# Performance work log

Hardware: AMD Instinct MI355X
Metric: run time of the kernel (lower is better)

The kernel has to match this reference:

```python
import math
import jax, jax.numpy as jnp
import numpy as np

B, N, M, C, H = 64, 64, 64, 512, 8
HD = C // H
FREQ = 256  # frequency_embedding_size
MAX_PERIOD = 10000.0


def setup_inputs() -> dict:
    key = jax.random.key(0)
    ks = jax.random.split(key, 10)
    s = 1.0 / math.sqrt(C)
    sf = 1.0 / math.sqrt(FREQ)
    return {
        "query": jax.random.normal(ks[0], (B, N, C), jnp.float32),
        "query_pos": jax.random.uniform(ks[1], (1, N, M), jnp.float32),
        # projection weights stored as [in, out]
        "Wq": jax.random.normal(ks[2], (C, C), jnp.float32) * s,
        "bq": jnp.zeros((C,), jnp.float32),
        "Wk": jax.random.normal(ks[3], (C, C), jnp.float32) * s,  # no bias
        "Wv": jax.random.normal(ks[4], (C, C), jnp.float32) * s,
        "bv": jnp.zeros((C,), jnp.float32),
        "Wo": jax.random.normal(ks[5], (C, C), jnp.float32) * s,
        "bo": jnp.zeros((C,), jnp.float32),
        # ScalarEmbedder MLP: Linear(FREQ->C), SiLU, Linear(C->C)
        "W1": jax.random.normal(ks[6], (FREQ, C), jnp.float32) * sf,
        "b1": jnp.zeros((C,), jnp.float32),
        "W2": jax.random.normal(ks[7], (C, C), jnp.float32) * s,
        "b2": jnp.zeros((C,), jnp.float32),
    }


def _freqs():
    half = FREQ // 2
    return jnp.exp(-math.log(MAX_PERIOD) * jnp.arange(half, dtype=jnp.float32) / half)


def reference(query, query_pos, Wq, bq, Wk, Wv, bv, Wo, bo, W1, b1, W2, b2):
    Bq, Nq, Cq = query.shape
    Mk = query_pos.shape[-1]
    # --- ScalarEmbedder on flattened pairwise positions: [N*M] -> [N*M, C]
    t = query_pos.reshape(-1)                       # [Bp*N*M], Bp = 1
    tf = t[:, None] * _freqs()[None, :]             # [N*M, FREQ/2]
    emb = jnp.concatenate([jnp.cos(tf), jnp.sin(tf)], axis=-1)  # [N*M, FREQ]
    pe = jax.nn.silu(emb @ W1 + b1) @ W2 + b2        # [N*M, C]
    pe = pe.reshape(Nq, Mk, H, HD).transpose(2, 0, 1, 3)  # [H, N, M, hd] (tiled over B via broadcast)

    q = (query @ Wq + bq).reshape(Bq, Nq, H, HD)     # bnhd
    k = (query @ Wk).reshape(Bq, Mk, H, HD)          # bmhd (key = query)
    v = (query @ Wv + bv).reshape(Bq, Mk, H, HD)

    scale = HD ** -0.5
    # attn[b,h,n,m] = sum_d q[b,n,h,d] * pe[h,n,m,d] * k[b,m,h,d]
    scores = jnp.einsum("bnhd,hnmd,bmhd->bhnm", q, pe, k) * scale
    attn = jax.nn.softmax(scores, axis=-1)
    x = jnp.einsum("bhnm,bmhd->bnhd", attn, v).reshape(Bq, Nq, Cq)
    return x @ Wo + bo + query  # identity = query
```

## Files before the change

kernel.cpp:

```cpp
#include <hip/hip_runtime.h>
#include <hip/hip_bf16.h>
#include <math.h>

typedef short short8 __attribute__((ext_vector_type(8)));
typedef float floatx4 __attribute__((ext_vector_type(4)));

__device__ __forceinline__ ushort f2bf(float f) {
    __hip_bfloat16 h = __float2bfloat16(f);
    return *reinterpret_cast<ushort*>(&h);
}
__device__ __forceinline__ void bf8_to_f32(uint4 u, float* f) {
    f[0] = __uint_as_float(u.x << 16); f[1] = __uint_as_float(u.x & 0xffff0000u);
    f[2] = __uint_as_float(u.y << 16); f[3] = __uint_as_float(u.y & 0xffff0000u);
    f[4] = __uint_as_float(u.z << 16); f[5] = __uint_as_float(u.z & 0xffff0000u);
    f[6] = __uint_as_float(u.w << 16); f[7] = __uint_as_float(u.w & 0xffff0000u);
}

#define GLDS16(g, l) __builtin_amdgcn_global_load_lds( \
    (const __attribute__((address_space(1))) void*)(g), \
    (__attribute__((address_space(3))) void*)(l), 16, 0, 0)

__global__ __launch_bounds__(256) void prep_kernel(
        const float* __restrict__ W1, const float* __restrict__ W2,
        const float* __restrict__ Wq, const float* __restrict__ Wk,
        const float* __restrict__ Wv, const float* __restrict__ Wo,
        const float* __restrict__ bq, const float* __restrict__ bv,
        const float* __restrict__ query, const float* __restrict__ qpos,
        ushort* __restrict__ W1t, ushort* __restrict__ W2t,
        ushort* __restrict__ Wqkvt, ushort* __restrict__ Wot,
        ushort* __restrict__ queryB, ushort* __restrict__ embB,
        float* __restrict__ biasC) {
    const int z = blockIdx.z;
    const int tx = threadIdx.x, ty = threadIdx.y;
    const int tid = ty * 32 + tx;
    if (z < 6) {
        const float* src; ushort* dst; int R;
        switch (z) {
            case 0:  src = W1; dst = W1t;              R = 256; break;
            case 1:  src = W2; dst = W2t;              R = 512; break;
            case 2:  src = Wq; dst = Wqkvt;            R = 512; break;
            case 3:  src = Wk; dst = Wqkvt + 512*512;  R = 512; break;
            case 4:  src = Wv; dst = Wqkvt + 1024*512; R = 512; break;
            default: src = Wo; dst = Wot;              R = 512; break;
        }
        const int r0 = blockIdx.y * 32, c0 = blockIdx.x * 32;
        if (r0 >= R) return;
        __shared__ float t[32][33];
        for (int i = ty; i < 32; i += 8) t[i][tx] = src[(size_t)(r0 + i) * 512 + c0 + tx];
        __syncthreads();
        for (int i = ty; i < 32; i += 8) dst[(size_t)(c0 + i) * R + r0 + tx] = f2bf(t[tx][i]);
    } else if (z == 6) {
        const int bid = blockIdx.y * 16 + blockIdx.x;
#pragma unroll
        for (int i = 0; i < 8; ++i) {
            size_t idx4 = (size_t)bid * 2048 + i * 256 + tid;
            float4 v = *(const float4*)(query + idx4 * 4);
            ushort4 o; o.x = f2bf(v.x); o.y = f2bf(v.y); o.z = f2bf(v.z); o.w = f2bf(v.w);
            *(ushort4*)(queryB + idx4 * 4) = o;
        }
        if (bid == 0) {
            for (int i = tid; i < 1536; i += 256)
                biasC[i] = (i < 512) ? bq[i] : ((i < 1024) ? 0.0f : bv[i - 1024]);
        }
    } else {
        const int bid = blockIdx.y * 16 + blockIdx.x;
        const int gt = bid * 256 + tid;
        const int e0 = gt * 16;
        const int r = e0 >> 8, j0 = e0 & 255;
        const float t = qpos[r];
        ushort o[16];
#pragma unroll
        for (int u = 0; u < 16; ++u) {
            int j = j0 + u, i = j & 127;
            float freq = __expf(-9.210340371976184f * (float)i * (1.0f / 128.0f));
            float a = t * freq;
            o[u] = f2bf((j < 128) ? __cosf(a) : __sinf(a));
        }
        *(uint4*)(embB + e0)     = *(uint4*)&o[0];
        *(uint4*)(embB + e0 + 8) = *(uint4*)&o[8];
    }
}

struct GArgs {
    const ushort* A; const ushort* Bt; const float* bias; const float* resid;
    void* C; int N, K, act, outf32, ntn;
};

template<int BM, int BN>
__global__ __launch_bounds__(256) void gemm_multi(GArgs g0, GArgs g1, int split) {
    constexpr int MR = BM / 32;
    constexpr int NR = BN / 32;
    __shared__ ushort As[2][BM * 32];
    __shared__ ushort Bs[2][BN * 32];

    const bool sel = ((int)blockIdx.x >= split);
    const GArgs g = sel ? g1 : g0;
    const int bid = sel ? ((int)blockIdx.x - split) : (int)blockIdx.x;
    const int tm = bid / g.ntn, tn = bid % g.ntn;
    const int row0 = tm * BM, col0 = tn * BN;
    const int K = g.K, N = g.N;

    const int tid = threadIdx.x;
    const int l = tid & 63, w = tid >> 6;
    const int wr = w >> 1, wc = w & 1;
    const int l15 = l & 15, quad = l >> 4;

    const int srow = tid >> 2;
    const int skoff = (tid & 3) * 8;
    const ushort* gA = g.A  + (size_t)(row0 + srow) * K + skoff;
    const ushort* gB = g.Bt + (size_t)(col0 + srow) * K + skoff;

    auto stage = [&](int s, int k0) {
#pragma unroll
        for (int i = 0; i < BM / 64; ++i)
            GLDS16(gA + (size_t)(i * 64) * K + k0, &As[s][(i * 256 + tid) * 8]);
#pragma unroll
        for (int i = 0; i < BN / 64; ++i)
            GLDS16(gB + (size_t)(i * 64) * K + k0, &Bs[s][(i * 256 + tid) * 8]);
    };

    floatx4 acc[MR][NR] = {};

    const int nk = K >> 5;
    stage(0, 0);
    int cur = 0;
    for (int t = 0; t < nk; ++t) {
        __syncthreads();
        if (t + 1 < nk) stage(cur ^ 1, (t + 1) * 32);
        short8 af[MR], bf[NR];
#pragma unroll
        for (int m = 0; m < MR; ++m)
            af[m] = *(const short8*)&As[cur][(wr * (BM / 2) + m * 16 + l15) * 32 + quad * 8];
#pragma unroll
        for (int n = 0; n < NR; ++n)
            bf[n] = *(const short8*)&Bs[cur][(wc * (BN / 2) + n * 16 + l15) * 32 + quad * 8];
#pragma unroll
        for (int m = 0; m < MR; ++m)
#pragma unroll
            for (int n = 0; n < NR; ++n)
                acc[m][n] = __builtin_amdgcn_mfma_f32_16x16x32_bf16(af[m], bf[n], acc[m][n], 0, 0, 0);
        cur ^= 1;
    }

#pragma unroll
    for (int m = 0; m < MR; ++m)
#pragma unroll
        for (int n = 0; n < NR; ++n) {
            int col = col0 + wc * (BN / 2) + n * 16 + l15;
            float bvv = g.bias ? g.bias[col] : 0.0f;
#pragma unroll
            for (int r = 0; r < 4; ++r) {
                int row = row0 + wr * (BM / 2) + m * 16 + quad * 4 + r;
                float val = acc[m][n][r] + bvv;
                if (g.act) val = val / (1.0f + __expf(-val));
                if (g.outf32) {
                    float rv = g.resid ? g.resid[(size_t)row * N + col] : 0.0f;
                    ((float*)g.C)[(size_t)row * N + col] = val + rv;
                } else {
                    ((ushort*)g.C)[(size_t)row * N + col] = f2bf(val);
                }
            }
        }
}

__global__ __launch_bounds__(256) void attn_bf16(
        const ushort* __restrict__ qkv, const ushort* __restrict__ peB,
        ushort* __restrict__ xB) {
    constexpr int PT = 72;
    const int h = blockIdx.x, b = blockIdx.y, nh = blockIdx.z;
    const int tid = threadIdx.x;
    const int w = tid >> 6, l = tid & 63;
    const int lo = l & 7, hi = l >> 3;
    const int l15 = l & 15, quad = l >> 4;

    __shared__ ushort vsT[64 * PT];
    __shared__ ushort ps[32 * PT];

    {
        const int rp = tid >> 3, ch = tid & 7;
        const ushort* vb = qkv + (size_t)(b * 64 + 2 * rp) * 1536 + h * 64 + 1024 + ch * 8;
        uint4 v0 = *(const uint4*)vb;
        uint4 v1 = *(const uint4*)(vb + 1536);
        const ushort* a0 = (const ushort*)&v0;
        const ushort* a1 = (const ushort*)&v1;
#pragma unroll
        for (int j = 0; j < 8; ++j) {
            uint pk = (uint)a0[j] | ((uint)a1[j] << 16);
            *(uint*)&vsT[(ch * 8 + j) * PT + 2 * rp] = pk;
        }
    }

    short8 ku[8];
#pragma unroll
    for (int mg = 0; mg < 8; ++mg)
        ku[mg] = *(const short8*)(qkv + (size_t)(b * 64 + mg * 8 + hi) * 1536 + h * 64 + 512 + lo * 8);

    for (int i = 0; i < 8; ++i) {
        int nl = w + 4 * i;
        int n = nh * 32 + nl;

        uint4 qu = *(const uint4*)(qkv + (size_t)(b * 64 + n) * 1536 + h * 64 + lo * 8);
        float qf[8]; bf8_to_f32(qu, qf);

        uint4 pu[8];
#pragma unroll
        for (int mg = 0; mg < 8; ++mg)
            pu[mg] = *(const uint4*)(peB + (size_t)(n * 64 + mg * 8 + hi) * 512 + h * 64 + lo * 8);

        float sreg[8];
#pragma unroll
        for (int mg = 0; mg < 8; ++mg) {
            float pf[8]; bf8_to_f32(pu[mg], pf);
            const ushort* kk = (const ushort*)&ku[mg];
            float p = 0.0f;
#pragma unroll
            for (int j = 0; j < 8; ++j) {
                float kfj = __uint_as_float(((uint)kk[j]) << 16);
                p = fmaf(qf[j] * kfj, pf[j], p);
            }
            p += __shfl_xor(p, 1);
            p += __shfl_xor(p, 2);
            p += __shfl_xor(p, 4);
            sreg[mg] = p * 0.125f;
        }

        float mx = sreg[0];
#pragma unroll
        for (int mg = 1; mg < 8; ++mg) mx = fmaxf(mx, sreg[mg]);
        mx = fmaxf(mx, __shfl_xor(mx, 8));
        mx = fmaxf(mx, __shfl_xor(mx, 16));
        mx = fmaxf(mx, __shfl_xor(mx, 32));
        float sum = 0.0f;
#pragma unroll
        for (int mg = 0; mg < 8; ++mg) { sreg[mg] = __expf(sreg[mg] - mx); sum += sreg[mg]; }
        sum += __shfl_xor(sum, 8);
        sum += __shfl_xor(sum, 16);
        sum += __shfl_xor(sum, 32);
        float rs = 1.0f / sum;

        float pv = sreg[0];
#pragma unroll
        for (int mg = 1; mg < 8; ++mg) if (lo == mg) pv = sreg[mg];
        ps[nl * PT + 8 * lo + hi] = f2bf(pv * rs);
    }
    __syncthreads();

    {
        const int ntile = w & 1;
        const int dt0 = (w >> 1) << 1;
        floatx4 o0 = {0.f, 0.f, 0.f, 0.f};
        floatx4 o1 = {0.f, 0.f, 0.f, 0.f};
#pragma unroll
        for (int ks = 0; ks < 2; ++ks) {
            short8 a  = *(const short8*)&ps[(ntile * 16 + l15) * PT + ks * 32 + quad * 8];
            short8 b0 = *(const short8*)&vsT[((dt0    ) * 16 + l15) * PT + ks * 32 + quad * 8];
            short8 b1 = *(const short8*)&vsT[((dt0 + 1) * 16 + l15) * PT + ks * 32 + quad * 8];
            o0 = __builtin_amdgcn_mfma_f32_16x16x32_bf16(a, b0, o0, 0, 0, 0);
            o1 = __builtin_amdgcn_mfma_f32_16x16x32_bf16(a, b1, o1, 0, 0, 0);
        }
        const int nbase = nh * 32 + ntile * 16 + quad * 4;
#pragma unroll
        for (int r = 0; r < 4; ++r) {
            size_t rowoff = (size_t)(b * 64 + nbase + r) * 512 + h * 64;
            xB[rowoff + (dt0    ) * 16 + l15] = f2bf(o0[r]);
            xB[rowoff + (dt0 + 1) * 16 + l15] = f2bf(o1[r]);
        }
    }
}

extern "C" void kernel_launch(void* const* d_in, const int* in_sizes, int n_in,
                              void* d_out, int out_size, void* d_ws, size_t ws_size,
                              hipStream_t stream) {
    const float* query = (const float*)d_in[0];
    const float* qpos  = (const float*)d_in[1];
    const float* Wq    = (const float*)d_in[2];
    const float* bq    = (const float*)d_in[3];
    const float* Wk    = (const float*)d_in[4];
    const float* Wv    = (const float*)d_in[5];
    const float* bv    = (const float*)d_in[6];
    const float* Wo    = (const float*)d_in[7];
    const float* bo    = (const float*)d_in[8];
    const float* W1    = (const float*)d_in[9];
    const float* b1    = (const float*)d_in[10];
    const float* W2    = (const float*)d_in[11];
    const float* b2    = (const float*)d_in[12];
    float* out = (float*)d_out;
    char* ws = (char*)d_ws;

    ushort* W1t    = (ushort*)(ws + 0);
    ushort* W2t    = (ushort*)(ws + 262144);
    ushort* Wqkvt  = (ushort*)(ws + 786432);
    ushort* Wot    = (ushort*)(ws + 2359296);
    float*  biasC  = (float*) (ws + 2883584);
    ushort* embB   = (ushort*)(ws + 3145728);
    ushort* queryB = (ushort*)(ws + 5242880);
    ushort* hiddenB= (ushort*)(ws + 9437184);
    ushort* peB    = (ushort*)(ws + 13631488);
    ushort* qkvB   = (ushort*)(ws + 17825792);
    ushort* xB     = (ushort*)(ws + 30408704);

    prep_kernel<<<dim3(16, 16, 8), dim3(32, 8), 0, stream>>>(
        W1, W2, Wq, Wk, Wv, Wo, bq, bv, query, qpos,
        W1t, W2t, Wqkvt, Wot, queryB, embB, biasC);

    GArgs a_g1 { embB,    W1t,   b1,    nullptr, hiddenB, 512,  256, 1, 0, 8  };
    GArgs a_g2 { hiddenB, W2t,   b2,    nullptr, peB,     512,  512, 0, 0, 8  };
    GArgs a_qkv{ queryB,  Wqkvt, biasC, nullptr, qkvB,    1536, 512, 0, 0, 24 };
    GArgs a_out{ xB,      Wot,   bo,    query,   out,     512,  512, 0, 1, 8  };

    gemm_multi<64, 64><<<512, 256, 0, stream>>>(a_g1, a_g1, 1 << 30);
    gemm_multi<64, 64><<<2048, 256, 0, stream>>>(a_g2, a_qkv, 512);

    attn_bf16<<<dim3(8, 64, 2), 256, 0, stream>>>(qkvB, peB, xB);

    gemm_multi<64, 64><<<512, 256, 0, stream>>>(a_out, a_out, 1 << 30);
}
```

Before: 158.0 us.

## Process two batches per attention block to reuse positional-embedding loads

Each attention block now handles two batch elements, so every positional-embedding tile loaded from global memory is used for two batches instead of one, halving pe traffic. K is staged in shared memory per batch instead of held in registers, and the grid's batch dimension is halved to match. Shared memory use roughly triples and the grid shrinks to 512 blocks, which may lower occupancy and parallelism.

New measurement: 168.7 us. 6.7% more time.

```diff
diff --git a/kernel.cpp b/kernel.cpp
--- a/kernel.cpp
+++ b/kernel.cpp
@@ -167,94 +167,110 @@
         const ushort* __restrict__ qkv, const ushort* __restrict__ peB,
         ushort* __restrict__ xB) {
     constexpr int PT = 72;
-    const int h = blockIdx.x, b = blockIdx.y, nh = blockIdx.z;
+    const int h = blockIdx.x, bp = blockIdx.y, nh = blockIdx.z;
     const int tid = threadIdx.x;
     const int w = tid >> 6, l = tid & 63;
     const int lo = l & 7, hi = l >> 3;
     const int l15 = l & 15, quad = l >> 4;
 
-    __shared__ ushort vsT[64 * PT];
-    __shared__ ushort ps[32 * PT];
-
-    {
-        const int rp = tid >> 3, ch = tid & 7;
-        const ushort* vb = qkv + (size_t)(b * 64 + 2 * rp) * 1536 + h * 64 + 1024 + ch * 8;
-        uint4 v0 = *(const uint4*)vb;
-        uint4 v1 = *(const uint4*)(vb + 1536);
-        const ushort* a0 = (const ushort*)&v0;
-        const ushort* a1 = (const ushort*)&v1;
-#pragma unroll
-        for (int j = 0; j < 8; ++j) {
-            uint pk = (uint)a0[j] | ((uint)a1[j] << 16);
-            *(uint*)&vsT[(ch * 8 + j) * PT + 2 * rp] = pk;
-        }
-    }
-
-    short8 ku[8];
-#pragma unroll
-    for (int mg = 0; mg < 8; ++mg)
-        ku[mg] = *(const short8*)(qkv + (size_t)(b * 64 + mg * 8 + hi) * 1536 + h * 64 + 512 + lo * 8);
+    __shared__ ushort kls[2][64 * PT];
+    __shared__ ushort vsT[2][64 * PT];
+    __shared__ ushort ps [2][32 * PT];
+
+#pragma unroll
+    for (int bb = 0; bb < 2; ++bb) {
+        const int b = bp * 2 + bb;
+        {
+            const int row = tid >> 2, c4 = tid & 3;
+            const ushort* kb = qkv + (size_t)(b * 64 + row) * 1536 + h * 64 + 512 + c4 * 16;
+            uint4 k0 = *(const uint4*)kb;
+            uint4 k1 = *(const uint4*)(kb + 8);
+            *(uint4*)&kls[bb][row * PT + c4 * 16]     = k0;
+            *(uint4*)&kls[bb][row * PT + c4 * 16 + 8] = k1;
+        }
+        {
+            const int rp = tid >> 3, ch = tid & 7;
+            const ushort* vb = qkv + (size_t)(b * 64 + 2 * rp) * 1536 + h * 64 + 1024 + ch * 8;
+            uint4 v0 = *(const uint4*)vb;
+            uint4 v1 = *(const uint4*)(vb + 1536);
+            const ushort* a0 = (const ushort*)&v0;
+            const ushort* a1 = (const ushort*)&v1;
+#pragma unroll
+            for (int j = 0; j < 8; ++j) {
+                uint pk = (uint)a0[j] | ((uint)a1[j] << 16);
+                *(uint*)&vsT[bb][(ch * 8 + j) * PT + 2 * rp] = pk;
+            }
+        }
+    }
+    __syncthreads();
 
     for (int i = 0; i < 8; ++i) {
         int nl = w + 4 * i;
         int n = nh * 32 + nl;
 
-        uint4 qu = *(const uint4*)(qkv + (size_t)(b * 64 + n) * 1536 + h * 64 + lo * 8);
-        float qf[8]; bf8_to_f32(qu, qf);
-
         uint4 pu[8];
 #pragma unroll
         for (int mg = 0; mg < 8; ++mg)
             pu[mg] = *(const uint4*)(peB + (size_t)(n * 64 + mg * 8 + hi) * 512 + h * 64 + lo * 8);
 
-        float sreg[8];
-#pragma unroll
-        for (int mg = 0; mg < 8; ++mg) {
-            float pf[8]; bf8_to_f32(pu[mg], pf);
-            const ushort* kk = (const ushort*)&ku[mg];
-            float p = 0.0f;
-#pragma unroll
-            for (int j = 0; j < 8; ++j) {
-                float kfj = __uint_as_float(((uint)kk[j]) << 16);
-                p = fmaf(qf[j] * kfj, pf[j], p);
+#pragma unroll
+        for (int bb = 0; bb < 2; ++bb) {
+            const int b = bp * 2 + bb;
+            uint4 qu = *(const uint4*)(qkv + (size_t)(b * 64 + n) * 1536 + h * 64 + lo * 8);
+            float qf[8]; bf8_to_f32(qu, qf);
+
+            float sreg[8];
+#pragma unroll
+            for (int mg = 0; mg < 8; ++mg) {
+                float pf[8]; bf8_to_f32(pu[mg], pf);
+                short8 kk = *(const short8*)&kls[bb][(mg * 8 + hi) * PT + lo * 8];
+                const ushort* kp = (const ushort*)&kk;
+                float p = 0.0f;
+#pragma unroll
+                for (int j = 0; j < 8; ++j) {
+                    float kfj = __uint_as_float(((uint)kp[j]) << 16);
+                    p = fmaf(qf[j] * kfj, pf[j], p);
+                }
+                p += __shfl_xor(p, 1);
+                p += __shfl_xor(p, 2);
+                p += __shfl_xor(p, 4);
+                sreg[mg] = p * 0.125f;
             }
-            p += __shfl_xor(p, 1);
-            p += __shfl_xor(p, 2);
-            p += __shfl_xor(p, 4);
-            sreg[mg] = p * 0.125f;
-        }
-
-        float mx = sreg[0];
-#pragma unroll
-        for (int mg = 1; mg < 8; ++mg) mx = fmaxf(mx, sreg[mg]);
-        mx = fmaxf(mx, __shfl_xor(mx, 8));
-        mx = fmaxf(mx, __shfl_xor(mx, 16));
-        mx = fmaxf(mx, __shfl_xor(mx, 32));
-        float sum = 0.0f;
-#pragma unroll
-        for (int mg = 0; mg < 8; ++mg) { sreg[mg] = __expf(sreg[mg] - mx); sum += sreg[mg]; }
-        sum += __shfl_xor(sum, 8);
-        sum += __shfl_xor(sum, 16);
-        sum += __shfl_xor(sum, 32);
-        float rs = 1.0f / sum;
-
-        float pv = sreg[0];
-#pragma unroll
-        for (int mg = 1; mg < 8; ++mg) if (lo == mg) pv = sreg[mg];
-        ps[nl * PT + 8 * lo + hi] = f2bf(pv * rs);
+
+            float mx = sreg[0];
+#pragma unroll
+            for (int mg = 1; mg < 8; ++mg) mx = fmaxf(mx, sreg[mg]);
+            mx = fmaxf(mx, __shfl_xor(mx, 8));
+            mx = fmaxf(mx, __shfl_xor(mx, 16));
+            mx = fmaxf(mx, __shfl_xor(mx, 32));
+            float sum = 0.0f;
+#pragma unroll
+            for (int mg = 0; mg < 8; ++mg) { sreg[mg] = __expf(sreg[mg] - mx); sum += sreg[mg]; }
+            sum += __shfl_xor(sum, 8);
+            sum += __shfl_xor(sum, 16);
+            sum += __shfl_xor(sum, 32);
+            float rs = 1.0f / sum;
+
+            float pv = sreg[0];
+#pragma unroll
+            for (int mg = 1; mg < 8; ++mg) if (lo == mg) pv = sreg[mg];
+            ps[bb][nl * PT + 8 * lo + hi] = f2bf(pv * rs);
+        }
     }
     __syncthreads();
 
-    {
+#pragma unroll
+    for (int bb = 0; bb < 2; ++bb) {
+        const int b = bp * 2 + bb;
         const int ntile = w & 1;
         const int dt0 = (w >> 1) << 1;
         floatx4 o0 = {0.f, 0.f, 0.f, 0.f};
         floatx4 o1 = {0.f, 0.f, 0.f, 0.f};
 #pragma unroll
-        for (int ks = 0; ks < 2; ++ks) {
-            short8 a  = *(const short8*)&ps[(ntile * 16 + l15) * PT + ks * 32 + quad * 8];
-            short8 b0 = *(const short8*)&vsT[((dt0    ) * 16 + l15) * PT + ks * 32 + quad * 8];
-            short8 b1 = *(const short8*)&vsT[((dt0 + 1) * 16 + l15) * PT + ks * 32 + quad * 8];
+        for (int kk = 0; kk < 2; ++kk) {
+            short8 a  = *(const short8*)&ps[bb][(ntile * 16 + l15) * PT + kk * 32 + quad * 8];
+            short8 b0 = *(const short8*)&vsT[bb][((dt0    ) * 16 + l15) * PT + kk * 32 + quad * 8];
+            short8 b1 = *(const short8*)&vsT[bb][((dt0 + 1) * 16 + l15) * PT + kk * 32 + quad * 8];
             o0 = __builtin_amdgcn_mfma_f32_16x16x32_bf16(a, b0, o0, 0, 0, 0);
             o1 = __builtin_amdgcn_mfma_f32_16x16x32_bf16(a, b1, o1, 0, 0, 0);
         }
@@ -311,7 +327,7 @@
     gemm_multi<64, 64><<<512, 256, 0, stream>>>(a_g1, a_g1, 1 << 30);
     gemm_multi<64, 64><<<2048, 256, 0, stream>>>(a_g2, a_qkv, 512);
 
-    attn_bf16<<<dim3(8, 64, 2), 256, 0, stream>>>(qkvB, peB, xB);
+    attn_bf16<<<dim3(8, 32, 2), 256, 0, stream>>>(qkvB, peB, xB);
 
     gemm_multi<64, 64><<<512, 256, 0, stream>>>(a_out, a_out, 1 << 30);
 }
```
